# Optimization experiments

Measured on AMD Instinct MI355X. Metric: run time of the kernel, lower is better.

Reference implementation:

```python
import jax, jax.numpy as jnp
import numpy as np

B = 8
A = 1614
TOPN = 6
IOU_THR = 0.25
PAD = 224
OUT = 224

def _make_anchors():
    # 6 anchor shapes on the 14x14 map, 6 on 7x7, 9 on 4x4 -> 1614 total,
    # ordered anchor-type-major then row-major spatial to match the [C,H,W] flatten
    # of the tidy conv outputs (as generate_default_anchor_maps does in NTS-Net).
    specs = [
        (14, 32.0, [(48, 48), (64, 48), (48, 64), (80, 80), (96, 64), (64, 96)]),
        (7, 64.0, [(96, 96), (128, 96), (96, 128), (160, 160), (192, 128), (128, 192)]),
        (4, 112.0, [(192, 192), (256, 192), (192, 256), (288, 288), (320, 256), (256, 320), (352, 352), (384, 320), (320, 384)]),
    ]
    blocks = []
    for fm, stride, sizes in specs:
        c = (np.arange(fm) + 0.5) * stride
        cy, cx = np.meshgrid(c, c, indexing='ij')
        for (h, w) in sizes:
            blocks.append(np.stack([cy - h / 2, cx - w / 2, cy + h / 2, cx + w / 2], -1).reshape(-1, 4))
    a = (np.concatenate(blocks, 0) + PAD).astype(np.int64)  # mimic (edge_anchors+224).astype(int)
    return a.astype(np.float32)  # [1614,4] (y0,x0,y1,x1) in padded-image coords

def _conv(x, w, b, stride, pad):
    y = jax.lax.conv_general_dilated(x, w, (stride, stride), [(pad, pad), (pad, pad)],
                                     dimension_numbers=('NCHW', 'OIHW', 'NCHW'))
    return y + b[None, :, None, None]

def _rpn_scores(rpn, wd1, bd1, wd2, bd2, wd3, bd3, wt1, bt1, wt2, bt2, wt3, bt3):
    b = rpn.shape[0]
    d1 = jax.nn.relu(_conv(rpn, wd1, bd1, 1, 1))   # [B,128,14,14]
    d2 = jax.nn.relu(_conv(d1, wd2, bd2, 2, 1))    # [B,128,7,7]
    d3 = jax.nn.relu(_conv(d2, wd3, bd3, 2, 1))    # [B,128,4,4]
    t1 = _conv(d1, wt1, bt1, 1, 0).reshape(b, -1)  # [B,1176]
    t2 = _conv(d2, wt2, bt2, 1, 0).reshape(b, -1)  # [B,294]
    t3 = _conv(d3, wt3, bt3, 1, 0).reshape(b, -1)  # [B,144]
    return jnp.concatenate([t1, t2, t3], axis=1)   # [B,1614]

def _nms_keep(boxes, scores):
    # Greedy NMS over all A anchors; returns keep mask in ORIGINAL anchor order.
    order = jnp.argsort(-scores)
    b = boxes[order]
    y0, x0, y1, x1 = b[:, 0], b[:, 1], b[:, 2], b[:, 3]
    area = (y1 - y0) * (x1 - x0)
    ih = jnp.clip(jnp.minimum(y1[:, None], y1[None, :]) - jnp.maximum(y0[:, None], y0[None, :]), 0)
    iw = jnp.clip(jnp.minimum(x1[:, None], x1[None, :]) - jnp.maximum(x0[:, None], x0[None, :]), 0)
    inter = ih * iw
    iou = inter / (area[:, None] + area[None, :] - inter)
    idx = jnp.arange(A)
    def body(i, supp):
        row = (iou[i] > IOU_THR) & (idx > i)
        return jnp.where(supp[i], supp, supp | row)
    supp = jax.lax.fori_loop(0, A, body, jnp.zeros((A,), bool))
    return jnp.zeros((A,), bool).at[order].set(~supp)

def _crop_resize(img, box):
    # img [3,Hp,Wp]; box int32 (x0,y0,x1,y1).
    # Equivalent to F.interpolate(img[:, y0:y1, x0:x1], (224,224), 'bilinear', align_corners=True)
    x0, y0, x1, y1 = box[0], box[1], box[2], box[3]
    t = jnp.arange(OUT, dtype=jnp.float32) / (OUT - 1)
    sy = y0.astype(jnp.float32) + t * (y1 - 1 - y0).astype(jnp.float32)
    sx = x0.astype(jnp.float32) + t * (x1 - 1 - x0).astype(jnp.float32)
    y0i = jnp.floor(sy).astype(jnp.int32); x0i = jnp.floor(sx).astype(jnp.int32)
    y1i = jnp.minimum(y0i + 1, y1 - 1);    x1i = jnp.minimum(x0i + 1, x1 - 1)
    wy = (sy - y0i.astype(jnp.float32))[None, :, None]
    wx = (sx - x0i.astype(jnp.float32))[None, None, :]
    g = lambda yi, xi: img[:, yi][:, :, xi]  # gather rows then cols -> [3,224,224]
    top = (1 - wx) * g(y0i, x0i) + wx * g(y0i, x1i)
    bot = (1 - wx) * g(y1i, x0i) + wx * g(y1i, x1i)
    return (1 - wy) * top + wy * bot

def setup_inputs():
    key = jax.random.key(0)
    ks = jax.random.split(key, 16)
    n = jax.random.normal
    return {
        'x': n(ks[0], (B, 3, 448, 448), jnp.float32),
        'rpn_feature': n(ks[1], (B, 2048, 14, 14), jnp.float32),
        'anchors': jnp.asarray(_make_anchors()),
        'wd1': 0.02 * n(ks[2], (128, 2048, 3, 3), jnp.float32), 'bd1': 0.01 * n(ks[3], (128,), jnp.float32),
        'wd2': 0.05 * n(ks[4], (128, 128, 3, 3), jnp.float32),  'bd2': 0.01 * n(ks[5], (128,), jnp.float32),
        'wd3': 0.05 * n(ks[6], (128, 128, 3, 3), jnp.float32),  'bd3': 0.01 * n(ks[7], (128,), jnp.float32),
        'wt1': 0.1 * n(ks[8], (6, 128, 1, 1), jnp.float32),     'bt1': 0.01 * n(ks[9], (6,), jnp.float32),
        'wt2': 0.1 * n(ks[10], (6, 128, 1, 1), jnp.float32),    'bt2': 0.01 * n(ks[11], (6,), jnp.float32),
        'wt3': 0.1 * n(ks[12], (9, 128, 1, 1), jnp.float32),    'bt3': 0.01 * n(ks[13], (9,), jnp.float32),
    }

def reference(x, rpn_feature, anchors, wd1, bd1, wd2, bd2, wd3, bd3, wt1, bt1, wt2, bt2, wt3, bt3):
    scores = _rpn_scores(rpn_feature, wd1, bd1, wd2, bd2, wd3, bd3, wt1, bt1, wt2, bt2, wt3, bt3)
    keep = jax.vmap(lambda s: _nms_keep(anchors, s))(scores)           # [B,A] bool
    masked = jnp.where(keep, scores, -jnp.inf)
    top_prob, top_idx = jax.lax.top_k(masked, TOPN)                    # [B,6]
    tb = anchors[top_idx]                                              # [B,6,4] (y0,x0,y1,x1)
    coords = jnp.stack([tb[..., 1], tb[..., 0], tb[..., 3], tb[..., 2]], -1)  # (x0,y0,x1,y1)
    x_pad = jnp.pad(x, ((0, 0), (0, 0), (PAD, PAD), (PAD, PAD)))       # [B,3,896,896]
    bint = coords.astype(jnp.int32)
    part_imgs = jax.vmap(lambda img, bs: jax.vmap(lambda bb: _crop_resize(img, bb))(bs))(x_pad, bint)  # [B,6,3,224,224]
    return part_imgs, coords, top_prob, top_idx
```

## Files before the change

kernel.cpp:

```cpp
#include <hip/hip_runtime.h>
#include <hip/hip_bf16.h>
#include <math.h>
#include <stdint.h>


#define OFF_COORDS 7225344
#define OFF_PROB   7225536
#define OFF_IDX    7225584
#define NA 1614
#define K1TOT 18432

typedef __attribute__((ext_vector_type(8)))  short  short8;
typedef __attribute__((ext_vector_type(16))) float  floatx16;

__global__ __launch_bounds__(256) void k_prep_a(const float* __restrict__ rpn,
                                                __hip_bfloat16* __restrict__ ah,
                                                __hip_bfloat16* __restrict__ al)
{
    __shared__ float tile[64][65];
    const int cib  = blockIdx.x * 64;
    const int posb = blockIdx.y * 64;
    const int b    = blockIdx.z;
    const int t    = threadIdx.x;
#pragma unroll
    for (int it = 0; it < 16; ++it) {
        int idx  = it * 256 + t;
        int cil  = idx >> 6;
        int posl = idx & 63;
        int pos  = posb + posl;
        int py = pos >> 4, px = pos & 15;
        int y = py - 1, x = px - 1;
        float v = 0.0f;
        if ((unsigned)y < 14u && (unsigned)x < 14u)
            v = rpn[((size_t)(b * 2048 + cib + cil) * 14 + y) * 14 + x];
        tile[cil][posl] = v;
    }
    __syncthreads();
#pragma unroll
    for (int it = 0; it < 16; ++it) {
        int idx  = it * 256 + t;
        int posl = idx >> 6;
        int cil  = idx & 63;
        float v = tile[cil][posl];
        __hip_bfloat16 h = __float2bfloat16(v);
        __hip_bfloat16 l = __float2bfloat16(v - __bfloat162float(h));
        size_t o = (size_t)(b * 256 + posb + posl) * 2048 + cib + cil;
        ah[o] = h; al[o] = l;
    }
}

__global__ __launch_bounds__(256) void k_prep_b(const float* __restrict__ w,
                                                __hip_bfloat16* __restrict__ bh,
                                                __hip_bfloat16* __restrict__ bl)
{
    const int tap = blockIdx.x;
    const int co  = blockIdx.y;
    const int t   = threadIdx.x;
#pragma unroll
    for (int i = 0; i < 8; ++i) {
        int ci = i * 256 + t;
        float v = w[((size_t)co * 2048 + ci) * 9 + tap];
        __hip_bfloat16 h = __float2bfloat16(v);
        __hip_bfloat16 l = __float2bfloat16(v - __bfloat162float(h));
        size_t o = (size_t)co * K1TOT + tap * 2048 + ci;
        bh[o] = h; bl[o] = l;
    }
}

__global__ __launch_bounds__(128) void k_prep_w23(const float* __restrict__ w2,
                                                  const float* __restrict__ w3,
                                                  __hip_bfloat16* __restrict__ b2h,
                                                  __hip_bfloat16* __restrict__ b2l,
                                                  __hip_bfloat16* __restrict__ b3h,
                                                  __hip_bfloat16* __restrict__ b3l)
{
    const int tap = blockIdx.x;
    const int co  = blockIdx.y;
    const int z   = blockIdx.z;
    const int ci  = threadIdx.x;
    const float* w = z ? w3 : w2;
    __hip_bfloat16* bh = z ? b3h : b2h;
    __hip_bfloat16* bl = z ? b3l : b2l;
    float v = w[((size_t)co * 128 + ci) * 9 + tap];
    __hip_bfloat16 h = __float2bfloat16(v);
    __hip_bfloat16 l = __float2bfloat16(v - __bfloat162float(h));
    size_t o = (size_t)co * 1152 + tap * 128 + ci;
    bh[o] = h; bl[o] = l;
}

template<int POSN, int OW, int STR, int CIN, int MTOT>
__global__ __launch_bounds__(256) void k_conv_mfma(const short* __restrict__ ah,
                                                   const short* __restrict__ al,
                                                   const short* __restrict__ bh,
                                                   const short* __restrict__ bl,
                                                   float* __restrict__ partial,
                                                   int chunk)
{
    constexpr int KTOT = CIN * 9;
    __shared__ short AsH[128][40];
    __shared__ short AsL[128][40];
    __shared__ short BsH[128][40];
    __shared__ short BsL[128][40];

    const int t     = threadIdx.x;
    const int lane  = t & 63;
    const int w     = t >> 6;
    const int wm    = (w & 1) * 64;
    const int wn    = (w >> 1) * 64;
    const int lm    = lane & 31;
    const int half  = lane >> 5;
    const int mbase = blockIdx.x * 128;
    const int k0    = blockIdx.y * chunk;
    const int k1    = (k0 + chunk < KTOT) ? (k0 + chunk) : KTOT;

    int arow[2], apos[2]; bool aval[2];
    const int akc = (t & 3) * 8;
#pragma unroll
    for (int i = 0; i < 2; ++i) {
        int row = ((i * 256 + t) >> 2);
        int m   = mbase + row;
        arow[i] = row;
        aval[i] = (m < MTOT);
        int mm = aval[i] ? m : 0;
        int b  = mm / POSN;
        int p  = mm - b * POSN;
        int y  = p / OW;
        int x  = p - y * OW;
        apos[i] = b * 256 + y * STR * 16 + x * STR;
    }

    floatx16 acc[2][2];
#pragma unroll
    for (int mf = 0; mf < 2; ++mf)
#pragma unroll
        for (int nf = 0; nf < 2; ++nf)
#pragma unroll
            for (int r = 0; r < 16; ++r) acc[mf][nf][r] = 0.0f;

    const short8 zero8 = {0, 0, 0, 0, 0, 0, 0, 0};

    for (int ks = k0; ks < k1; ks += 32) {
        const int tap = ks / CIN;
        const int ci0 = ks - tap * CIN;
        const int dy  = tap / 3, dx = tap - dy * 3;
#pragma unroll
        for (int i = 0; i < 2; ++i) {
            short8 vh = zero8, vl = zero8;
            if (aval[i]) {
                size_t g = (size_t)(apos[i] + dy * 16 + dx) * CIN + ci0 + akc;
                vh = *(const short8*)(ah + g);
                vl = *(const short8*)(al + g);
            }
            *(short8*)&AsH[arow[i]][akc] = vh;
            *(short8*)&AsL[arow[i]][akc] = vl;
        }
#pragma unroll
        for (int i = 0; i < 2; ++i) {
            int n = ((i * 256 + t) >> 2);
            size_t g = (size_t)n * KTOT + ks + akc;
            *(short8*)&BsH[n][akc] = *(const short8*)(bh + g);
            *(short8*)&BsL[n][akc] = *(const short8*)(bl + g);
        }
        __syncthreads();
#pragma unroll
        for (int kst = 0; kst < 2; ++kst) {
            const int koff = kst * 16 + half * 8;
            short8 a_h[2], a_l[2], b_h[2], b_l[2];
#pragma unroll
            for (int mf = 0; mf < 2; ++mf) {
                a_h[mf] = *(const short8*)&AsH[wm + mf * 32 + lm][koff];
                a_l[mf] = *(const short8*)&AsL[wm + mf * 32 + lm][koff];
            }
#pragma unroll
            for (int nf = 0; nf < 2; ++nf) {
                b_h[nf] = *(const short8*)&BsH[wn + nf * 32 + lm][koff];
                b_l[nf] = *(const short8*)&BsL[wn + nf * 32 + lm][koff];
            }
#pragma unroll
            for (int mf = 0; mf < 2; ++mf)
#pragma unroll
                for (int nf = 0; nf < 2; ++nf) {
                    acc[mf][nf] = __builtin_amdgcn_mfma_f32_32x32x16_bf16(
                        a_h[mf], b_h[nf], acc[mf][nf], 0, 0, 0);
                    acc[mf][nf] = __builtin_amdgcn_mfma_f32_32x32x16_bf16(
                        a_h[mf], b_l[nf], acc[mf][nf], 0, 0, 0);
                    acc[mf][nf] = __builtin_amdgcn_mfma_f32_32x32x16_bf16(
                        a_l[mf], b_h[nf], acc[mf][nf], 0, 0, 0);
                }
        }
        __syncthreads();
    }

    float* P = partial + (size_t)blockIdx.y * MTOT * 128;
#pragma unroll
    for (int mf = 0; mf < 2; ++mf)
#pragma unroll
        for (int nf = 0; nf < 2; ++nf)
#pragma unroll
            for (int r = 0; r < 16; ++r) {
                int row = (r & 3) + 8 * (r >> 2) + 4 * half;
                int m = mbase + wm + mf * 32 + row;
                int n = wn + nf * 32 + lm;
                if (m < MTOT) P[(size_t)m * 128 + n] = acc[mf][nf][r];
            }
}

template<int POSN, int OWV>
__global__ __launch_bounds__(256) void k_reduce_pad(const float* __restrict__ partial,
                                                    const float* __restrict__ bias,
                                                    float* __restrict__ dn,
                                                    __hip_bfloat16* __restrict__ ph,
                                                    __hip_bfloat16* __restrict__ pl,
                                                    int S)
{
    constexpr int MTOT = 8 * POSN;
    int idx = blockIdx.x * 256 + threadIdx.x;
    int b   = idx >> 15;
    int pos = (idx >> 7) & 255;
    int co  = idx & 127;
    int y = (pos >> 4) - 1;
    int x = (pos & 15) - 1;
    if ((unsigned)y < (unsigned)OWV && (unsigned)x < (unsigned)OWV) {
        int m = b * POSN + y * OWV + x;
        float s = bias[co];
        for (int k = 0; k < S; ++k) s += partial[(size_t)k * MTOT * 128 + m * 128 + co];
        s = fmaxf(s, 0.0f);
        dn[(size_t)m * 128 + co] = s;
        __hip_bfloat16 h = __float2bfloat16(s);
        __hip_bfloat16 l = __float2bfloat16(s - __bfloat162float(h));
        ph[idx] = h; pl[idx] = l;
    } else {
        ph[idx] = __float2bfloat16(0.0f);
        pl[idx] = __float2bfloat16(0.0f);
    }
}

__global__ __launch_bounds__(256) void k_reduce3(const float* __restrict__ partial,
                                                 const float* __restrict__ bias,
                                                 float* __restrict__ dn, int S)
{
    int idx = blockIdx.x * 256 + threadIdx.x;
    int co  = idx & 127;
    float s = bias[co];
    for (int k = 0; k < S; ++k) s += partial[(size_t)k * 128 * 128 + idx];
    dn[idx] = fmaxf(s, 0.0f);
}

__global__ __launch_bounds__(256) void k_heads(const float* __restrict__ d1n,
                                               const float* __restrict__ d2n,
                                               const float* __restrict__ d3n,
                                               const float* __restrict__ w1, const float* __restrict__ b1,
                                               const float* __restrict__ w2, const float* __restrict__ b2,
                                               const float* __restrict__ w3, const float* __restrict__ b3,
                                               float* __restrict__ scores)
{
    int idx = blockIdx.x * 256 + threadIdx.x;
    if (idx >= 8 * NA) return;
    int b = idx / NA;
    int e = idx - b * NA;
    const float* d; const float* w; float bias;
    if (e < 1176) {
        int c = e / 196, p = e - c * 196;
        d = d1n + (size_t)(b * 196 + p) * 128; w = w1 + c * 128; bias = b1[c];
    } else if (e < 1470) {
        int e2 = e - 1176; int c = e2 / 49, p = e2 - c * 49;
        d = d2n + (size_t)(b * 49 + p) * 128; w = w2 + c * 128; bias = b2[c];
    } else {
        int e2 = e - 1470; int c = e2 / 16, p = e2 - c * 16;
        d = d3n + (size_t)(b * 16 + p) * 128; w = w3 + c * 128; bias = b3[c];
    }
    float s = bias;
#pragma unroll
    for (int i = 0; i < 32; ++i) {
        float4 dv = ((const float4*)d)[i];
        float4 wv = ((const float4*)w)[i];
        s = fmaf(dv.x, wv.x, s);
        s = fmaf(dv.y, wv.y, s);
        s = fmaf(dv.z, wv.z, s);
        s = fmaf(dv.w, wv.w, s);
    }
    scores[idx] = s;
}

__global__ __launch_bounds__(256) void k_nms_topk(const float* __restrict__ scores,
                                                  const float* __restrict__ anchors,
                                                  float* __restrict__ out,
                                                  int* __restrict__ boxes)
{
    __shared__ float ms[NA];
    __shared__ float ay0[NA], ax0[NA], ay1[NA], ax1[NA];
    __shared__ unsigned char picked[NA];
    __shared__ float rv[4]; __shared__ int ri[4];
    __shared__ float win[5];
    int b = blockIdx.x;
    int t = threadIdx.x;
    for (int i = t; i < NA; i += 256) {
        ms[i] = scores[b * NA + i];
        float4 an = ((const float4*)anchors)[i];
        ay0[i] = an.x; ax0[i] = an.y; ay1[i] = an.z; ax1[i] = an.w;
        picked[i] = 0;
    }
    __syncthreads();
    for (int r = 0; r < 6; ++r) {
        float bv = -INFINITY; int bi = NA;
        for (int i = t; i < NA; i += 256) {
            if (!picked[i]) {
                float v = ms[i];
                if (v > bv || (v == bv && i < bi)) { bv = v; bi = i; }
            }
        }
#pragma unroll
        for (int off = 32; off > 0; off >>= 1) {
            float v2 = __shfl_down(bv, off);
            int   i2 = __shfl_down(bi, off);
            if (v2 > bv || (v2 == bv && i2 < bi)) { bv = v2; bi = i2; }
        }
        if ((t & 63) == 0) { rv[t >> 6] = bv; ri[t >> 6] = bi; }
        __syncthreads();
        if (t == 0) {
            bv = rv[0]; bi = ri[0];
            for (int wv = 1; wv < 4; ++wv)
                if (rv[wv] > bv || (rv[wv] == bv && ri[wv] < bi)) { bv = rv[wv]; bi = ri[wv]; }
            picked[bi] = 1;
            win[0] = ay0[bi]; win[1] = ax0[bi]; win[2] = ay1[bi]; win[3] = ax1[bi]; win[4] = bv;
            int o = b * 6 + r;
            out[OFF_COORDS + o * 4 + 0] = ax0[bi];
            out[OFF_COORDS + o * 4 + 1] = ay0[bi];
            out[OFF_COORDS + o * 4 + 2] = ax1[bi];
            out[OFF_COORDS + o * 4 + 3] = ay1[bi];
            out[OFF_PROB + o] = bv;
            out[OFF_IDX  + o] = (float)bi;
            boxes[o * 4 + 0] = (int)ax0[bi];
            boxes[o * 4 + 1] = (int)ay0[bi];
            boxes[o * 4 + 2] = (int)ax1[bi];
            boxes[o * 4 + 3] = (int)ay1[bi];
        }
        __syncthreads();
        float by0 = win[0], bx0 = win[1], by1 = win[2], bx1 = win[3];
        float barea = (by1 - by0) * (bx1 - bx0);
        for (int i = t; i < NA; i += 256) {
            if (picked[i]) continue;
            float ih = fmaxf(fminf(by1, ay1[i]) - fmaxf(by0, ay0[i]), 0.0f);
            float iw = fmaxf(fminf(bx1, ax1[i]) - fmaxf(bx0, ax0[i]), 0.0f);
            float inter = ih * iw;
            float area  = (ay1[i] - ay0[i]) * (ax1[i] - ax0[i]);
            float iou = inter / (barea + area - inter);
            if (iou > 0.25f) ms[i] = -INFINITY;
        }
        __syncthreads();
    }
}

__global__ __launch_bounds__(256) void k_crop(const float* __restrict__ x,
                                              const int* __restrict__ boxes,
                                              float* __restrict__ out)
{
    int bid = blockIdx.x;
    int i = threadIdx.x;
    if (i >= 224) return;
    int j   = bid % 224;
    int rem = bid / 224;
    int c   = rem % 3;
    int br  = rem / 3;
    int b   = br / 6;
    int4 bx = ((const int4*)boxes)[br];
    float tj = (float)j / 223.0f;
    float sy = (float)bx.y + tj * (float)(bx.w - 1 - bx.y);
    int y0i = (int)floorf(sy);
    int y1i = min(y0i + 1, bx.w - 1);
    float wy = sy - (float)y0i;
    float ti = (float)i / 223.0f;
    float sx = (float)bx.x + ti * (float)(bx.z - 1 - bx.x);
    int x0i = (int)floorf(sx);
    int x1i = min(x0i + 1, bx.z - 1);
    float wx = sx - (float)x0i;
    const float* img = x + ((size_t)b * 3 + c) * 448 * 448;
    auto g = [&](int yy, int xx) -> float {
        yy -= 224; xx -= 224;
        if ((unsigned)yy >= 448u || (unsigned)xx >= 448u) return 0.0f;
        return img[(size_t)yy * 448 + xx];
    };
    float g00 = g(y0i, x0i), g01 = g(y0i, x1i);
    float g10 = g(y1i, x0i), g11 = g(y1i, x1i);
    float top = (1.0f - wx) * g00 + wx * g01;
    float bot = (1.0f - wx) * g10 + wx * g11;
    out[(size_t)bid * 224 + i] = (1.0f - wy) * top + wy * bot;
}

extern "C" void kernel_launch(void* const* d_in, const int* in_sizes, int n_in,
                              void* d_out, int out_size, void* d_ws, size_t ws_size,
                              hipStream_t stream)
{
    (void)in_sizes; (void)n_in; (void)out_size;
    const float* x    = (const float*)d_in[0];
    const float* rpn  = (const float*)d_in[1];
    const float* anch = (const float*)d_in[2];
    const float* wd1  = (const float*)d_in[3];
    const float* bd1  = (const float*)d_in[4];
    const float* wd2  = (const float*)d_in[5];
    const float* bd2  = (const float*)d_in[6];
    const float* wd3  = (const float*)d_in[7];
    const float* bd3  = (const float*)d_in[8];
    const float* hw1  = (const float*)d_in[9];
    const float* hb1  = (const float*)d_in[10];
    const float* hw2  = (const float*)d_in[11];
    const float* hb2  = (const float*)d_in[12];
    const float* hw3  = (const float*)d_in[13];
    const float* hb3  = (const float*)d_in[14];
    float* out = (float*)d_out;

    char* ws = (char*)d_ws;
    size_t off = 0;
    auto alloc = [&](size_t bytes) -> void* {
        void* p = ws + off;
        off = (off + bytes + 255) & ~(size_t)255;
        return p;
    };
    __hip_bfloat16* ahb  = (__hip_bfloat16*)alloc((size_t)8 * 256 * 2048 * 2);
    __hip_bfloat16* alb  = (__hip_bfloat16*)alloc((size_t)8 * 256 * 2048 * 2);
    __hip_bfloat16* b1h  = (__hip_bfloat16*)alloc((size_t)128 * K1TOT * 2);
    __hip_bfloat16* b1l  = (__hip_bfloat16*)alloc((size_t)128 * K1TOT * 2);
    __hip_bfloat16* b2h  = (__hip_bfloat16*)alloc((size_t)128 * 1152 * 2);
    __hip_bfloat16* b2l  = (__hip_bfloat16*)alloc((size_t)128 * 1152 * 2);
    __hip_bfloat16* b3h  = (__hip_bfloat16*)alloc((size_t)128 * 1152 * 2);
    __hip_bfloat16* b3l  = (__hip_bfloat16*)alloc((size_t)128 * 1152 * 2);
    __hip_bfloat16* d1ph = (__hip_bfloat16*)alloc((size_t)8 * 256 * 128 * 2);
    __hip_bfloat16* d1pl = (__hip_bfloat16*)alloc((size_t)8 * 256 * 128 * 2);
    __hip_bfloat16* d2ph = (__hip_bfloat16*)alloc((size_t)8 * 256 * 128 * 2);
    __hip_bfloat16* d2pl = (__hip_bfloat16*)alloc((size_t)8 * 256 * 128 * 2);
    float* d1n  = (float*)alloc((size_t)8 * 196 * 128 * 4);
    float* d2n  = (float*)alloc((size_t)8 * 49 * 128 * 4);
    float* d3n  = (float*)alloc((size_t)8 * 16 * 128 * 4);
    float* sc   = (float*)alloc((size_t)8 * NA * 4);
    int*  boxes = (int*)alloc((size_t)8 * 6 * 4 * 4);
    size_t avail = (ws_size > off) ? (ws_size - off) : 0;
    float* P = (float*)(ws + off);

    long long s1 = (long long)(avail / ((size_t)1568 * 128 * 4));
    if (s1 > 48) s1 = 48;
    if (s1 < 1)  s1 = 1;
    int S1 = (int)s1;
    int chunk1 = ((K1TOT + S1 * 32 - 1) / (S1 * 32)) * 32;

    k_prep_b<<<dim3(9, 128), 256, 0, stream>>>(wd1, b1h, b1l);
    k_prep_w23<<<dim3(9, 128, 2), 128, 0, stream>>>(wd2, wd3, b2h, b2l, b3h, b3l);
    k_prep_a<<<dim3(32, 4, 8), 256, 0, stream>>>(rpn, ahb, alb);

    k_conv_mfma<196, 14, 1, 2048, 1568><<<dim3(13, S1), 256, 0, stream>>>(
        (const short*)ahb, (const short*)alb, (const short*)b1h, (const short*)b1l, P, chunk1);
    k_reduce_pad<196, 14><<<dim3(1024), 256, 0, stream>>>(P, bd1, d1n, d1ph, d1pl, S1);

    k_conv_mfma<49, 7, 2, 128, 392><<<dim3(4, 9), 256, 0, stream>>>(
        (const short*)d1ph, (const short*)d1pl, (const short*)b2h, (const short*)b2l, P, 128);
    k_reduce_pad<49, 7><<<dim3(1024), 256, 0, stream>>>(P, bd2, d2n, d2ph, d2pl, 9);

    k_conv_mfma<16, 4, 2, 128, 128><<<dim3(1, 9), 256, 0, stream>>>(
        (const short*)d2ph, (const short*)d2pl, (const short*)b3h, (const short*)b3l, P, 128);
    k_reduce3<<<dim3(64), 256, 0, stream>>>(P, bd3, d3n, 9);

    k_heads<<<dim3((8 * NA + 255) / 256), 256, 0, stream>>>(d1n, d2n, d3n,
        hw1, hb1, hw2, hb2, hw3, hb3, sc);
    k_nms_topk<<<dim3(8), 256, 0, stream>>>(sc, anch, out, boxes);
    k_crop<<<dim3(8 * 6 * 3 * 224), 256, 0, stream>>>(x, boxes, out);
}
```

Before: 260.8 us.

## Prefetch conv tiles into registers, remap blocks per XCD, vectorize reductions and weight prep

The MFMA conv kernel now loads the next K-slice into registers while the current slice is computed, so global loads overlap the matrix math. Grid launch is flattened to 1D, and blocks are remapped so that the K-chunks sharing an M tile land on the same XCD, aiming for better L2 reuse. The reduce kernels use float4 loads and stores with four channels per thread, and k_prep_b stages weights through shared memory for coalesced reads. Register prefetch raises register pressure, and the XCD mapping depends on the grid size being a multiple of 8*GX.

Result: no change. 256.1 us (-1.8%).

```diff
diff --git a/kernel.cpp b/kernel.cpp
--- a/kernel.cpp
+++ b/kernel.cpp
@@ -12,6 +12,15 @@
 
 typedef __attribute__((ext_vector_type(8)))  short  short8;
 typedef __attribute__((ext_vector_type(16))) float  floatx16;
+
+__device__ inline void split_bf16(float v, unsigned short& h, unsigned short& l)
+{
+    __hip_bfloat16 hb = __float2bfloat16(v);
+    float hv = __bfloat162float(hb);
+    __hip_bfloat16 lb = __float2bfloat16(v - hv);
+    h = *reinterpret_cast<unsigned short*>(&hb);
+    l = *reinterpret_cast<unsigned short*>(&lb);
+}
 
 __global__ __launch_bounds__(256) void k_prep_a(const float* __restrict__ rpn,
                                                 __hip_bfloat16* __restrict__ ah,
@@ -42,10 +51,11 @@
         int posl = idx >> 6;
         int cil  = idx & 63;
         float v = tile[cil][posl];
-        __hip_bfloat16 h = __float2bfloat16(v);
-        __hip_bfloat16 l = __float2bfloat16(v - __bfloat162float(h));
+        unsigned short h, l;
+        split_bf16(v, h, l);
         size_t o = (size_t)(b * 256 + posb + posl) * 2048 + cib + cil;
-        ah[o] = h; al[o] = l;
+        ((unsigned short*)ah)[o] = h;
+        ((unsigned short*)al)[o] = l;
     }
 }
 
@@ -53,17 +63,26 @@
                                                 __hip_bfloat16* __restrict__ bh,
                                                 __hip_bfloat16* __restrict__ bl)
 {
-    const int tap = blockIdx.x;
+    __shared__ float tile[9][260];
+    const int ci0 = blockIdx.x * 256;
     const int co  = blockIdx.y;
     const int t   = threadIdx.x;
-#pragma unroll
-    for (int i = 0; i < 8; ++i) {
-        int ci = i * 256 + t;
-        float v = w[((size_t)co * 2048 + ci) * 9 + tap];
-        __hip_bfloat16 h = __float2bfloat16(v);
-        __hip_bfloat16 l = __float2bfloat16(v - __bfloat162float(h));
-        size_t o = (size_t)co * K1TOT + tap * 2048 + ci;
-        bh[o] = h; bl[o] = l;
+    const float* wc = w + (size_t)co * K1TOT + (size_t)ci0 * 9;
+#pragma unroll
+    for (int it = 0; it < 9; ++it) {
+        int i = it * 256 + t;
+        float v = wc[i];
+        tile[i % 9][i / 9] = v;
+    }
+    __syncthreads();
+#pragma unroll
+    for (int tap = 0; tap < 9; ++tap) {
+        float v = tile[tap][t];
+        unsigned short h, l;
+        split_bf16(v, h, l);
+        size_t o = (size_t)co * K1TOT + (size_t)tap * 2048 + ci0 + t;
+        ((unsigned short*)bh)[o] = h;
+        ((unsigned short*)bl)[o] = l;
     }
 }
 
@@ -82,13 +101,14 @@
     __hip_bfloat16* bh = z ? b3h : b2h;
     __hip_bfloat16* bl = z ? b3l : b2l;
     float v = w[((size_t)co * 128 + ci) * 9 + tap];
-    __hip_bfloat16 h = __float2bfloat16(v);
-    __hip_bfloat16 l = __float2bfloat16(v - __bfloat162float(h));
+    unsigned short h, l;
+    split_bf16(v, h, l);
     size_t o = (size_t)co * 1152 + tap * 128 + ci;
-    bh[o] = h; bl[o] = l;
-}
-
-template<int POSN, int OW, int STR, int CIN, int MTOT>
+    ((unsigned short*)bh)[o] = h;
+    ((unsigned short*)bl)[o] = l;
+}
+
+template<int POSN, int OW, int STR, int CIN, int MTOT, int GX>
 __global__ __launch_bounds__(256) void k_conv_mfma(const short* __restrict__ ah,
                                                    const short* __restrict__ al,
                                                    const short* __restrict__ bh,
@@ -109,8 +129,22 @@
     const int wn    = (w >> 1) * 64;
     const int lm    = lane & 31;
     const int half  = lane >> 5;
-    const int mbase = blockIdx.x * 128;
-    const int k0    = blockIdx.y * chunk;
+
+    const int nb = gridDim.x;
+    const int id = blockIdx.x;
+    int mb, kc;
+    if ((nb % (8 * GX)) == 0) {
+        int xcd = id & 7;
+        int j   = id >> 3;
+        int jq  = j / GX;
+        mb = j - jq * GX;
+        kc = xcd + 8 * jq;
+    } else {
+        kc = id / GX;
+        mb = id - kc * GX;
+    }
+    const int mbase = mb * 128;
+    const int k0    = kc * chunk;
     const int k1    = (k0 + chunk < KTOT) ? (k0 + chunk) : KTOT;
 
     int arow[2], apos[2]; bool aval[2];
@@ -138,30 +172,45 @@
             for (int r = 0; r < 16; ++r) acc[mf][nf][r] = 0.0f;
 
     const short8 zero8 = {0, 0, 0, 0, 0, 0, 0, 0};
-
-    for (int ks = k0; ks < k1; ks += 32) {
+    short8 rAh[2], rAl[2], rBh[2], rBl[2];
+
+    auto stage_load = [&](int ks) {
         const int tap = ks / CIN;
         const int ci0 = ks - tap * CIN;
         const int dy  = tap / 3, dx = tap - dy * 3;
 #pragma unroll
         for (int i = 0; i < 2; ++i) {
-            short8 vh = zero8, vl = zero8;
             if (aval[i]) {
                 size_t g = (size_t)(apos[i] + dy * 16 + dx) * CIN + ci0 + akc;
-                vh = *(const short8*)(ah + g);
-                vl = *(const short8*)(al + g);
-            }
-            *(short8*)&AsH[arow[i]][akc] = vh;
-            *(short8*)&AsL[arow[i]][akc] = vl;
+                rAh[i] = *(const short8*)(ah + g);
+                rAl[i] = *(const short8*)(al + g);
+            } else { rAh[i] = zero8; rAl[i] = zero8; }
         }
 #pragma unroll
         for (int i = 0; i < 2; ++i) {
             int n = ((i * 256 + t) >> 2);
             size_t g = (size_t)n * KTOT + ks + akc;
-            *(short8*)&BsH[n][akc] = *(const short8*)(bh + g);
-            *(short8*)&BsL[n][akc] = *(const short8*)(bl + g);
+            rBh[i] = *(const short8*)(bh + g);
+            rBl[i] = *(const short8*)(bl + g);
+        }
+    };
+
+    if (k0 < k1) stage_load(k0);
+
+    for (int ks = k0; ks < k1; ks += 32) {
+#pragma unroll
+        for (int i = 0; i < 2; ++i) {
+            *(short8*)&AsH[arow[i]][akc] = rAh[i];
+            *(short8*)&AsL[arow[i]][akc] = rAl[i];
+        }
+#pragma unroll
+        for (int i = 0; i < 2; ++i) {
+            int n = ((i * 256 + t) >> 2);
+            *(short8*)&BsH[n][akc] = rBh[i];
+            *(short8*)&BsL[n][akc] = rBl[i];
         }
         __syncthreads();
+        if (ks + 32 < k1) stage_load(ks + 32);
 #pragma unroll
         for (int kst = 0; kst < 2; ++kst) {
             const int koff = kst * 16 + half * 8;
@@ -191,7 +240,7 @@
         __syncthreads();
     }
 
-    float* P = partial + (size_t)blockIdx.y * MTOT * 128;
+    float* P = partial + (size_t)kc * MTOT * 128;
 #pragma unroll
     for (int mf = 0; mf < 2; ++mf)
 #pragma unroll
@@ -215,23 +264,32 @@
 {
     constexpr int MTOT = 8 * POSN;
     int idx = blockIdx.x * 256 + threadIdx.x;
-    int b   = idx >> 15;
-    int pos = (idx >> 7) & 255;
-    int co  = idx & 127;
+    int b   = idx >> 13;
+    int pos = (idx >> 5) & 255;
+    int c4  = idx & 31;
     int y = (pos >> 4) - 1;
     int x = (pos & 15) - 1;
     if ((unsigned)y < (unsigned)OWV && (unsigned)x < (unsigned)OWV) {
         int m = b * POSN + y * OWV + x;
-        float s = bias[co];
-        for (int k = 0; k < S; ++k) s += partial[(size_t)k * MTOT * 128 + m * 128 + co];
-        s = fmaxf(s, 0.0f);
-        dn[(size_t)m * 128 + co] = s;
-        __hip_bfloat16 h = __float2bfloat16(s);
-        __hip_bfloat16 l = __float2bfloat16(s - __bfloat162float(h));
-        ph[idx] = h; pl[idx] = l;
+        float4 s = ((const float4*)bias)[c4];
+        for (int k = 0; k < S; ++k) {
+            float4 p = ((const float4*)(partial + (size_t)k * MTOT * 128 + (size_t)m * 128))[c4];
+            s.x += p.x; s.y += p.y; s.z += p.z; s.w += p.w;
+        }
+        s.x = fmaxf(s.x, 0.0f); s.y = fmaxf(s.y, 0.0f);
+        s.z = fmaxf(s.z, 0.0f); s.w = fmaxf(s.w, 0.0f);
+        ((float4*)dn)[(size_t)m * 32 + c4] = s;
+        ushort4 h, l;
+        split_bf16(s.x, h.x, l.x);
+        split_bf16(s.y, h.y, l.y);
+        split_bf16(s.z, h.z, l.z);
+        split_bf16(s.w, h.w, l.w);
+        ((ushort4*)ph)[idx] = h;
+        ((ushort4*)pl)[idx] = l;
     } else {
-        ph[idx] = __float2bfloat16(0.0f);
-        pl[idx] = __float2bfloat16(0.0f);
+        ushort4 z = {0, 0, 0, 0};
+        ((ushort4*)ph)[idx] = z;
+        ((ushort4*)pl)[idx] = z;
     }
 }
 
@@ -240,10 +298,15 @@
                                                  float* __restrict__ dn, int S)
 {
     int idx = blockIdx.x * 256 + threadIdx.x;
-    int co  = idx & 127;
-    float s = bias[co];
-    for (int k = 0; k < S; ++k) s += partial[(size_t)k * 128 * 128 + idx];
-    dn[idx] = fmaxf(s, 0.0f);
+    int c4  = idx & 31;
+    float4 s = ((const float4*)bias)[c4];
+    for (int k = 0; k < S; ++k) {
+        float4 p = ((const float4*)(partial + (size_t)k * 128 * 128))[idx];
+        s.x += p.x; s.y += p.y; s.z += p.z; s.w += p.w;
+    }
+    s.x = fmaxf(s.x, 0.0f); s.y = fmaxf(s.y, 0.0f);
+    s.z = fmaxf(s.z, 0.0f); s.w = fmaxf(s.w, 0.0f);
+    ((float4*)dn)[idx] = s;
 }
 
 __global__ __launch_bounds__(256) void k_heads(const float* __restrict__ d1n,
@@ -442,21 +505,21 @@
     int S1 = (int)s1;
     int chunk1 = ((K1TOT + S1 * 32 - 1) / (S1 * 32)) * 32;
 
-    k_prep_b<<<dim3(9, 128), 256, 0, stream>>>(wd1, b1h, b1l);
+    k_prep_b<<<dim3(8, 128), 256, 0, stream>>>(wd1, b1h, b1l);
     k_prep_w23<<<dim3(9, 128, 2), 128, 0, stream>>>(wd2, wd3, b2h, b2l, b3h, b3l);
     k_prep_a<<<dim3(32, 4, 8), 256, 0, stream>>>(rpn, ahb, alb);
 
-    k_conv_mfma<196, 14, 1, 2048, 1568><<<dim3(13, S1), 256, 0, stream>>>(
+    k_conv_mfma<196, 14, 1, 2048, 1568, 13><<<dim3(13 * S1), 256, 0, stream>>>(
         (const short*)ahb, (const short*)alb, (const short*)b1h, (const short*)b1l, P, chunk1);
-    k_reduce_pad<196, 14><<<dim3(1024), 256, 0, stream>>>(P, bd1, d1n, d1ph, d1pl, S1);
-
-    k_conv_mfma<49, 7, 2, 128, 392><<<dim3(4, 9), 256, 0, stream>>>(
+    k_reduce_pad<196, 14><<<dim3(256), 256, 0, stream>>>(P, bd1, d1n, d1ph, d1pl, S1);
+
+    k_conv_mfma<49, 7, 2, 128, 392, 4><<<dim3(36), 256, 0, stream>>>(
         (const short*)d1ph, (const short*)d1pl, (const short*)b2h, (const short*)b2l, P, 128);
-    k_reduce_pad<49, 7><<<dim3(1024), 256, 0, stream>>>(P, bd2, d2n, d2ph, d2pl, 9);
-
-    k_conv_mfma<16, 4, 2, 128, 128><<<dim3(1, 9), 256, 0, stream>>>(
+    k_reduce_pad<49, 7><<<dim3(256), 256, 0, stream>>>(P, bd2, d2n, d2ph, d2pl, 9);
+
+    k_conv_mfma<16, 4, 2, 128, 128, 1><<<dim3(9), 256, 0, stream>>>(
         (const short*)d2ph, (const short*)d2pl, (const short*)b3h, (const short*)b3l, P, 128);
-    k_reduce3<<<dim3(64), 256, 0, stream>>>(P, bd3, d3n, 9);
+    k_reduce3<<<dim3(16), 256, 0, stream>>>(P, bd3, d3n, 9);
 
     k_heads<<<dim3((8 * NA + 255) / 256), 256, 0, stream>>>(d1n, d2n, d3n,
         hw1, hb1, hw2, hb2, hw3, hb3, sc);
```
